# Kernel optimization log

Measured on AMD Instinct MI355X. Metric: run time of the kernel, lower is better.

Reference implementation:

```python
import jax, jax.numpy as jnp
import numpy as np


def setup_inputs() -> dict:
    key = jax.random.key(0)
    k1, k2, k3, k4, k5 = jax.random.split(key, 5)
    B, T, H_enc, H_dec, A = 64, 2048, 512, 512, 512
    scale_enc = float(np.sqrt(2.0 / (H_enc + A)))  # xavier_uniform-ish scale
    scale_dec = float(np.sqrt(2.0 / (H_dec + A)))
    scale_v = float(np.sqrt(2.0 / (A + 1)))
    return {
        "encoder_outputs": jax.random.normal(k1, (B, T, H_enc), dtype=jnp.float32),
        "decoder_hidden": jax.random.normal(k2, (B, H_dec), dtype=jnp.float32),
        "W_enc": jax.random.normal(k3, (A, H_enc), dtype=jnp.float32) * scale_enc,
        "W_dec": jax.random.normal(k4, (A, H_dec), dtype=jnp.float32) * scale_dec,
        "V": jax.random.normal(k5, (1, A), dtype=jnp.float32) * scale_v,
    }


def reference(encoder_outputs, decoder_hidden, W_enc, W_dec, V):
    # enc_proj: [B,T,A]; dec_proj: [B,1,A] broadcast-added
    enc_proj = jnp.einsum("bth,ah->bta", encoder_outputs, W_enc)
    dec_proj = jnp.einsum("bh,ah->ba", decoder_hidden, W_dec)[:, None, :]
    energy = jnp.tanh(enc_proj + dec_proj)                      # [B,T,A]
    scores = jnp.einsum("bta,a->bt", energy, V[0])              # [B,T]
    attention_weights = jax.nn.softmax(scores, axis=1)          # [B,T]
    context_vector = jnp.einsum("bt,bth->bh", attention_weights, encoder_outputs)
    return context_vector, attention_weights
```

## Files before the change

### kernel.cpp

```cpp
#include <hip/hip_runtime.h>

#define B_ 64
#define T_ 2048
#define H_ 512
#define A_ 512

typedef unsigned short u16;
typedef __attribute__((ext_vector_type(8))) short bf16x8;
typedef __attribute__((ext_vector_type(4))) float f32x4;

__device__ __forceinline__ u16 f2bf(float f) {
  unsigned u = __float_as_uint(f);
  unsigned r = (u + 0x7FFFu + ((u >> 16) & 1u)) >> 16;
  return (u16)r;
}

__device__ __forceinline__ float bf2f(u16 h) {
  return __uint_as_float(((unsigned)h) << 16);
}

__device__ __forceinline__ float fast_tanh(float x) {
  float e = __expf(2.0f * x);
  return 1.0f - 2.0f * __builtin_amdgcn_rcpf(e + 1.0f);
}

#define BAR_LDS() asm volatile("s_waitcnt lgkmcnt(0)\n\ts_barrier" ::: "memory")

__global__ void k_prep(const float* __restrict__ W, u16* __restrict__ wsB,
                       const float* __restrict__ dec, const float* __restrict__ Wd,
                       float* __restrict__ dp) {
  __shared__ float dl[H_];
  int tid = threadIdx.x;
  int bx = blockIdx.x;
  if (bx < 128) {
    int u = bx * 256 + tid;
    int a = u >> 6;
    int hq = u & 63;
    int ks = hq >> 2;
    int q = hq & 3;
    const float4* src = (const float4*)(W + a * H_ + hq * 8);
    float4 x0 = src[0], x1 = src[1];
    uint4 pk;
    pk.x = (unsigned)f2bf(x0.x) | ((unsigned)f2bf(x0.y) << 16);
    pk.y = (unsigned)f2bf(x0.z) | ((unsigned)f2bf(x0.w) << 16);
    pk.z = (unsigned)f2bf(x1.x) | ((unsigned)f2bf(x1.y) << 16);
    pk.w = (unsigned)f2bf(x1.z) | ((unsigned)f2bf(x1.w) << 16);
    int dst = ks * 2048 + (a >> 4) * 64 + q * 16 + (a & 15);
    ((uint4*)wsB)[dst] = pk;
  } else {
    int e = bx - 128;
    int b = e >> 3;
    int a0 = (e & 7) * 64;
    dl[tid] = dec[b * H_ + tid];
    dl[tid + 256] = dec[b * H_ + tid + 256];
    __syncthreads();
    int al = tid >> 2, p = tid & 3;
    const float4* wr = (const float4*)(Wd + (a0 + al) * H_ + p * 128);
    const float4* dv = (const float4*)(dl + p * 128);
    float s = 0.f;
#pragma unroll 8
    for (int i = 0; i < 32; ++i) {
      float4 w4 = wr[i], d4 = dv[i];
      s += w4.x * d4.x + w4.y * d4.y + w4.z * d4.z + w4.w * d4.w;
    }
    s += __shfl_xor(s, 1);
    s += __shfl_xor(s, 2);
    if (p == 0) dp[b * H_ + a0 + al] = s;
  }
}

__launch_bounds__(512, 4)
__global__ void k_scores(const float* __restrict__ enc, const u16* __restrict__ wsB,
                         const float* __restrict__ dpj, const float* __restrict__ V,
                         float* __restrict__ scores, float* __restrict__ part,
                         float* __restrict__ mz) {
  __shared__ __attribute__((aligned(16))) u16 Ab[64 * 512];
  __shared__ float red[8][64];
  int tid = threadIdx.x;
  int w = tid >> 6, l = tid & 63;
  int q = l >> 4, r = l & 15;
  int m0 = blockIdx.x * 64;
  int b = m0 >> 11;

  int rem = tid & 255;
  int sm = rem >> 6, sq = (rem >> 4) & 3, sr = rem & 15;
  const float* ab = enc + (size_t)(m0 + sm * 16 + sr) * H_ + (tid >> 8) * 32 + sq * 8;

#define LOADC(y0, y1, y2, y3, c)                                      \
  {                                                                   \
    y0 = *((const float4*)(ab + (2 * (c)) * 64));                     \
    y1 = *((const float4*)(ab + (2 * (c)) * 64 + 4));                 \
    y2 = *((const float4*)(ab + (2 * (c) + 1) * 64));                 \
    y3 = *((const float4*)(ab + (2 * (c) + 1) * 64 + 4));             \
  }
#define STG_WRITE(y0, y1, it)                                         \
  {                                                                   \
    uint4 pk;                                                         \
    pk.x = (unsigned)f2bf(y0.x) | ((unsigned)f2bf(y0.y) << 16);       \
    pk.y = (unsigned)f2bf(y0.z) | ((unsigned)f2bf(y0.w) << 16);       \
    pk.z = (unsigned)f2bf(y1.x) | ((unsigned)f2bf(y1.y) << 16);       \
    pk.w = (unsigned)f2bf(y1.z) | ((unsigned)f2bf(y1.w) << 16);       \
    ((uint4*)Ab)[(it) * 512 + tid] = pk;                              \
  }
#define WRITEC(y0, y1, y2, y3, c)                                     \
  {                                                                   \
    STG_WRITE(y0, y1, 2 * (c))                                        \
    STG_WRITE(y2, y3, 2 * (c) + 1)                                    \
  }
#define COMPUTE4(c)                                                   \
  {                                                                   \
    _Pragma("unroll") for (int kk = 0; kk < 4; ++kk) {                \
      int ks = (c) * 4 + kk;                                          \
      bf16x8 bb[4], af[4];                                            \
      _Pragma("unroll") for (int n = 0; n < 4; ++n)                   \
          bb[n] = bfrag[ks * 2048 + (w * 4 + n) * 64 + l];            \
      _Pragma("unroll") for (int m = 0; m < 4; ++m)                   \
          af[m] = *((const bf16x8*)&Ab[(ks * 256 + m * 64 + l) * 8]); \
      __builtin_amdgcn_s_setprio(1);                                  \
      _Pragma("unroll") for (int m = 0; m < 4; ++m)                   \
          _Pragma("unroll") for (int n = 0; n < 4; ++n)               \
              acc[m][n] = __builtin_amdgcn_mfma_f32_16x16x32_bf16(    \
                  af[m], bb[n], acc[m][n], 0, 0, 0);                  \
      __builtin_amdgcn_s_setprio(0);                                  \
    }                                                                 \
  }

  f32x4 acc[4][4];
#pragma unroll
  for (int m = 0; m < 4; ++m)
#pragma unroll
    for (int n = 0; n < 4; ++n) acc[m][n] = (f32x4){0.f, 0.f, 0.f, 0.f};

  const bf16x8* bfrag = (const bf16x8*)wsB;

  float4 ya0, ya1, ya2, ya3, yb0, yb1, yb2, yb3;
  LOADC(ya0, ya1, ya2, ya3, 0)
  LOADC(yb0, yb1, yb2, yb3, 1)
  WRITEC(ya0, ya1, ya2, ya3, 0)
  BAR_LDS();
  LOADC(ya0, ya1, ya2, ya3, 2)
  COMPUTE4(0)
  WRITEC(yb0, yb1, yb2, yb3, 1)
  BAR_LDS();
  LOADC(yb0, yb1, yb2, yb3, 3)
  COMPUTE4(1)
  WRITEC(ya0, ya1, ya2, ya3, 2)
  BAR_LDS();
  COMPUTE4(2)
  WRITEC(yb0, yb1, yb2, yb3, 3)
  BAR_LDS();
  COMPUTE4(3)

  float sp[4][4] = {};
  const float* db = dpj + b * A_;
#pragma unroll
  for (int n = 0; n < 4; ++n) {
    int col = w * 64 + n * 16 + r;
    float vv = V[col];
    float dd = db[col];
#pragma unroll
    for (int m = 0; m < 4; ++m)
#pragma unroll
      for (int j = 0; j < 4; ++j)
        sp[m][j] = fmaf(vv, fast_tanh(acc[m][n][j] + dd), sp[m][j]);
  }
#pragma unroll
  for (int m = 0; m < 4; ++m)
#pragma unroll
    for (int j = 0; j < 4; ++j) {
      float v = sp[m][j];
      v += __shfl_xor(v, 1);
      v += __shfl_xor(v, 2);
      v += __shfl_xor(v, 4);
      v += __shfl_xor(v, 8);
      sp[m][j] = v;
    }
  float outv = 0.f;
#pragma unroll
  for (int mm = 0; mm < 4; ++mm)
#pragma unroll
    for (int jj = 0; jj < 4; ++jj)
      if (r == mm * 4 + jj) outv = sp[mm][jj];
  red[w][(r >> 2) * 16 + q * 4 + (r & 3)] = outv;
  BAR_LDS();

  float s = 0.f;
#pragma unroll
  for (int ww = 0; ww < 8; ++ww) s += red[ww][l];
  if (w == 0) scores[m0 + l] = s;
  float mx = s;
#pragma unroll
  for (int off = 1; off <= 32; off <<= 1) mx = fmaxf(mx, __shfl_xor(mx, off));
  float e = __expf(s - mx);
  float Z = e;
#pragma unroll
  for (int off = 1; off <= 32; off <<= 1) Z += __shfl_xor(Z, off);
  if (tid == 0) {
    mz[blockIdx.x * 2] = mx;
    mz[blockIdx.x * 2 + 1] = Z;
  }
  float em[4];
#pragma unroll
  for (int m = 0; m < 4; ++m) em[m] = __shfl(e, m * 16 + r);

  {
    float pv0[8], pv1[8];
#pragma unroll
    for (int j = 0; j < 8; ++j) { pv0[j] = 0.f; pv1[j] = 0.f; }
#pragma unroll
    for (int ksl = 0; ksl < 2; ++ksl) {
      int ks = 2 * w + ksl;
#pragma unroll
      for (int m = 0; m < 4; ++m) {
        uint4 pk = ((const uint4*)Ab)[ks * 256 + m * 64 + l];
        float er = em[m];
        float v0 = bf2f((u16)(pk.x & 0xffff)), v1 = bf2f((u16)(pk.x >> 16));
        float v2 = bf2f((u16)(pk.y & 0xffff)), v3 = bf2f((u16)(pk.y >> 16));
        float v4 = bf2f((u16)(pk.z & 0xffff)), v5 = bf2f((u16)(pk.z >> 16));
        float v6 = bf2f((u16)(pk.w & 0xffff)), v7 = bf2f((u16)(pk.w >> 16));
        if (ksl == 0) {
          pv0[0] = fmaf(er, v0, pv0[0]); pv0[1] = fmaf(er, v1, pv0[1]);
          pv0[2] = fmaf(er, v2, pv0[2]); pv0[3] = fmaf(er, v3, pv0[3]);
          pv0[4] = fmaf(er, v4, pv0[4]); pv0[5] = fmaf(er, v5, pv0[5]);
          pv0[6] = fmaf(er, v6, pv0[6]); pv0[7] = fmaf(er, v7, pv0[7]);
        } else {
          pv1[0] = fmaf(er, v0, pv1[0]); pv1[1] = fmaf(er, v1, pv1[1]);
          pv1[2] = fmaf(er, v2, pv1[2]); pv1[3] = fmaf(er, v3, pv1[3]);
          pv1[4] = fmaf(er, v4, pv1[4]); pv1[5] = fmaf(er, v5, pv1[5]);
          pv1[6] = fmaf(er, v6, pv1[6]); pv1[7] = fmaf(er, v7, pv1[7]);
        }
      }
    }
#pragma unroll
    for (int j = 0; j < 8; ++j) {
      float a0 = pv0[j], a1 = pv1[j];
      a0 += __shfl_xor(a0, 1); a1 += __shfl_xor(a1, 1);
      a0 += __shfl_xor(a0, 2); a1 += __shfl_xor(a1, 2);
      a0 += __shfl_xor(a0, 4); a1 += __shfl_xor(a1, 4);
      a0 += __shfl_xor(a0, 8); a1 += __shfl_xor(a1, 8);
      pv0[j] = a0; pv1[j] = a1;
    }
    float ov = 0.f;
#pragma unroll
    for (int jj = 0; jj < 8; ++jj) {
      if (r == jj) ov = pv0[jj];
      if (r == jj + 8) ov = pv1[jj];
    }
    int col = w * 64 + (r >> 3) * 32 + q * 8 + (r & 7);
    part[(size_t)blockIdx.x * 512 + col] = ov;
  }
#undef LOADC
#undef STG_WRITE
#undef WRITEC
#undef COMPUTE4
}

__global__ void k_softmax(const float* __restrict__ scores, float* __restrict__ wts) {
  __shared__ float rm[4], rs[4];
  int b = blockIdx.x, tid = threadIdx.x;
  float s[8];
#pragma unroll
  for (int i = 0; i < 8; ++i) s[i] = scores[b * T_ + i * 256 + tid];
  float mx = s[0];
#pragma unroll
  for (int i = 1; i < 8; ++i) mx = fmaxf(mx, s[i]);
#pragma unroll
  for (int off = 1; off <= 32; off <<= 1) mx = fmaxf(mx, __shfl_xor(mx, off));
  if ((tid & 63) == 0) rm[tid >> 6] = mx;
  __syncthreads();
  mx = fmaxf(fmaxf(rm[0], rm[1]), fmaxf(rm[2], rm[3]));
  float ex[8], se = 0.f;
#pragma unroll
  for (int i = 0; i < 8; ++i) { ex[i] = __expf(s[i] - mx); se += ex[i]; }
#pragma unroll
  for (int off = 1; off <= 32; off <<= 1) se += __shfl_xor(se, off);
  if ((tid & 63) == 0) rs[tid >> 6] = se;
  __syncthreads();
  se = rs[0] + rs[1] + rs[2] + rs[3];
  float inv = 1.0f / se;
#pragma unroll
  for (int i = 0; i < 8; ++i) wts[b * T_ + i * 256 + tid] = ex[i] * inv;
}

__global__ void k_ctx_comb(const float* __restrict__ part, const float* __restrict__ mz,
                           float* __restrict__ ctx) {
  __shared__ float sM[32], sZ[32];
  int b = blockIdx.x, tid = threadIdx.x;
  if (tid < 32) {
    sM[tid] = mz[(b * 32 + tid) * 2];
    sZ[tid] = mz[(b * 32 + tid) * 2 + 1];
  }
  __syncthreads();
  float M = sM[0];
#pragma unroll
  for (int i = 1; i < 32; ++i) M = fmaxf(M, sM[i]);
  float denom = 0.f;
#pragma unroll
  for (int i = 0; i < 32; ++i) denom += sZ[i] * __expf(sM[i] - M);
  float s = 0.f;
#pragma unroll
  for (int i = 0; i < 32; ++i)
    s += part[((size_t)b * 32 + i) * 512 + tid] * __expf(sM[i] - M);
  ctx[b * 512 + tid] = s / denom;
}

extern "C" void kernel_launch(void* const* d_in, const int* in_sizes, int n_in,
                              void* d_out, int out_size, void* d_ws, size_t ws_size,
                              hipStream_t stream) {
  const float* enc  = (const float*)d_in[0];
  const float* dec  = (const float*)d_in[1];
  const float* Wenc = (const float*)d_in[2];
  const float* Wdec = (const float*)d_in[3];
  const float* V    = (const float*)d_in[4];
  float* out = (float*)d_out;
  char* ws = (char*)d_ws;

  u16* wsB      = (u16*)ws;
  float* dpj    = (float*)(ws + 512 * 1024);
  float* scores = (float*)(ws + 640 * 1024);
  float* part   = (float*)(ws + 1152 * 1024);
  float* mz     = (float*)(ws + 1152 * 1024 + 4 * 1024 * 1024);

  float* ctx = out;
  float* wts = out + B_ * H_;

  hipLaunchKernelGGL(k_prep, dim3(640), dim3(256), 0, stream, Wenc, wsB, dec, Wdec, dpj);
  hipLaunchKernelGGL(k_scores, dim3(2048), dim3(512), 0, stream, enc, wsB, dpj, V,
                     scores, part, mz);
  hipLaunchKernelGGL(k_softmax, dim3(64), dim3(256), 0, stream, scores, wts);
  hipLaunchKernelGGL(k_ctx_comb, dim3(64), dim3(512), 0, stream, part, mz, ctx);
}
```

Before: 122.0 us.

## Software-pipeline B fragment loads, use packed bf16 convert, butterfly reductions

The scores kernel now prefetches W fragments from global memory two k-steps ahead and interleaves LDS A loads with the MFMA groups, giving more register buffers per thread. The launch bound drops from 4 to 2 blocks per CU so the extra registers fit. Float-to-bf16 rounding now uses the hardware v_cvt_pk_bf16_f32 instruction instead of integer arithmetic, and tanh calls v_exp_f32 directly on a prescaled input. The shuffle reductions become recursive-halving butterflies, cutting the shuffle count at the cost of a permuted output index. The lower occupancy reduces the latency hiding available to the encoder streaming loads.

```diff
diff --git a/kernel.cpp b/kernel.cpp
--- a/kernel.cpp
+++ b/kernel.cpp
@@ -9,10 +9,10 @@
 typedef __attribute__((ext_vector_type(8))) short bf16x8;
 typedef __attribute__((ext_vector_type(4))) float f32x4;
 
-__device__ __forceinline__ u16 f2bf(float f) {
-  unsigned u = __float_as_uint(f);
-  unsigned r = (u + 0x7FFFu + ((u >> 16) & 1u)) >> 16;
-  return (u16)r;
+__device__ __forceinline__ unsigned cvtpk(float lo, float hi) {
+  unsigned d;
+  asm("v_cvt_pk_bf16_f32 %0, %1, %2" : "=v"(d) : "v"(lo), "v"(hi));
+  return d;
 }
 
 __device__ __forceinline__ float bf2f(u16 h) {
@@ -20,8 +20,9 @@
 }
 
 __device__ __forceinline__ float fast_tanh(float x) {
-  float e = __expf(2.0f * x);
-  return 1.0f - 2.0f * __builtin_amdgcn_rcpf(e + 1.0f);
+  float e2;
+  asm("v_exp_f32 %0, %1" : "=v"(e2) : "v"(x * 2.8853900817779268f));
+  return 1.0f - 2.0f * __builtin_amdgcn_rcpf(e2 + 1.0f);
 }
 
 #define BAR_LDS() asm volatile("s_waitcnt lgkmcnt(0)\n\ts_barrier" ::: "memory")
@@ -41,10 +42,10 @@
     const float4* src = (const float4*)(W + a * H_ + hq * 8);
     float4 x0 = src[0], x1 = src[1];
     uint4 pk;
-    pk.x = (unsigned)f2bf(x0.x) | ((unsigned)f2bf(x0.y) << 16);
-    pk.y = (unsigned)f2bf(x0.z) | ((unsigned)f2bf(x0.w) << 16);
-    pk.z = (unsigned)f2bf(x1.x) | ((unsigned)f2bf(x1.y) << 16);
-    pk.w = (unsigned)f2bf(x1.z) | ((unsigned)f2bf(x1.w) << 16);
+    pk.x = cvtpk(x0.x, x0.y);
+    pk.y = cvtpk(x0.z, x0.w);
+    pk.z = cvtpk(x1.x, x1.y);
+    pk.w = cvtpk(x1.z, x1.w);
     int dst = ks * 2048 + (a >> 4) * 64 + q * 16 + (a & 15);
     ((uint4*)wsB)[dst] = pk;
   } else {
@@ -69,7 +70,7 @@
   }
 }
 
-__launch_bounds__(512, 4)
+__launch_bounds__(512, 2)
 __global__ void k_scores(const float* __restrict__ enc, const u16* __restrict__ wsB,
                          const float* __restrict__ dpj, const float* __restrict__ V,
                          float* __restrict__ scores, float* __restrict__ part,
@@ -86,112 +87,123 @@
   int sm = rem >> 6, sq = (rem >> 4) & 3, sr = rem & 15;
   const float* ab = enc + (size_t)(m0 + sm * 16 + sr) * H_ + (tid >> 8) * 32 + sq * 8;
 
-#define LOADC(y0, y1, y2, y3, c)                                      \
-  {                                                                   \
-    y0 = *((const float4*)(ab + (2 * (c)) * 64));                     \
-    y1 = *((const float4*)(ab + (2 * (c)) * 64 + 4));                 \
-    y2 = *((const float4*)(ab + (2 * (c) + 1) * 64));                 \
-    y3 = *((const float4*)(ab + (2 * (c) + 1) * 64 + 4));             \
-  }
-#define STG_WRITE(y0, y1, it)                                         \
-  {                                                                   \
-    uint4 pk;                                                         \
-    pk.x = (unsigned)f2bf(y0.x) | ((unsigned)f2bf(y0.y) << 16);       \
-    pk.y = (unsigned)f2bf(y0.z) | ((unsigned)f2bf(y0.w) << 16);       \
-    pk.z = (unsigned)f2bf(y1.x) | ((unsigned)f2bf(y1.y) << 16);       \
-    pk.w = (unsigned)f2bf(y1.z) | ((unsigned)f2bf(y1.w) << 16);       \
-    ((uint4*)Ab)[(it) * 512 + tid] = pk;                              \
-  }
-#define WRITEC(y0, y1, y2, y3, c)                                     \
-  {                                                                   \
-    STG_WRITE(y0, y1, 2 * (c))                                        \
-    STG_WRITE(y2, y3, 2 * (c) + 1)                                    \
-  }
-#define COMPUTE4(c)                                                   \
-  {                                                                   \
-    _Pragma("unroll") for (int kk = 0; kk < 4; ++kk) {                \
-      int ks = (c) * 4 + kk;                                          \
-      bf16x8 bb[4], af[4];                                            \
-      _Pragma("unroll") for (int n = 0; n < 4; ++n)                   \
-          bb[n] = bfrag[ks * 2048 + (w * 4 + n) * 64 + l];            \
-      _Pragma("unroll") for (int m = 0; m < 4; ++m)                   \
-          af[m] = *((const bf16x8*)&Ab[(ks * 256 + m * 64 + l) * 8]); \
-      __builtin_amdgcn_s_setprio(1);                                  \
-      _Pragma("unroll") for (int m = 0; m < 4; ++m)                   \
-          _Pragma("unroll") for (int n = 0; n < 4; ++n)               \
-              acc[m][n] = __builtin_amdgcn_mfma_f32_16x16x32_bf16(    \
-                  af[m], bb[n], acc[m][n], 0, 0, 0);                  \
-      __builtin_amdgcn_s_setprio(0);                                  \
-    }                                                                 \
-  }
-
-  f32x4 acc[4][4];
-#pragma unroll
-  for (int m = 0; m < 4; ++m)
-#pragma unroll
-    for (int n = 0; n < 4; ++n) acc[m][n] = (f32x4){0.f, 0.f, 0.f, 0.f};
-
-  const bf16x8* bfrag = (const bf16x8*)wsB;
-
-  float4 ya0, ya1, ya2, ya3, yb0, yb1, yb2, yb3;
-  LOADC(ya0, ya1, ya2, ya3, 0)
-  LOADC(yb0, yb1, yb2, yb3, 1)
-  WRITEC(ya0, ya1, ya2, ya3, 0)
-  BAR_LDS();
-  LOADC(ya0, ya1, ya2, ya3, 2)
-  COMPUTE4(0)
-  WRITEC(yb0, yb1, yb2, yb3, 1)
-  BAR_LDS();
-  LOADC(yb0, yb1, yb2, yb3, 3)
-  COMPUTE4(1)
-  WRITEC(ya0, ya1, ya2, ya3, 2)
-  BAR_LDS();
-  COMPUTE4(2)
-  WRITEC(yb0, yb1, yb2, yb3, 3)
-  BAR_LDS();
-  COMPUTE4(3)
-
-  float sp[4][4] = {};
+  float vv[4], dd[4];
   const float* db = dpj + b * A_;
 #pragma unroll
   for (int n = 0; n < 4; ++n) {
     int col = w * 64 + n * 16 + r;
-    float vv = V[col];
-    float dd = db[col];
+    vv[n] = V[col];
+    dd[n] = db[col];
+  }
+
+  const bf16x8* bfrag = (const bf16x8*)wsB;
+
+#define LOADC(P, c)                                                     \
+  { P##0 = *((const float4*)(ab + (2 * (c)) * 64));                     \
+    P##1 = *((const float4*)(ab + (2 * (c)) * 64 + 4));                 \
+    P##2 = *((const float4*)(ab + (2 * (c) + 1) * 64));                 \
+    P##3 = *((const float4*)(ab + (2 * (c) + 1) * 64 + 4)); }
+#define WRITEC(P, c)                                                    \
+  { uint4 k0, k1;                                                       \
+    k0.x = cvtpk((P##0).x, (P##0).y); k0.y = cvtpk((P##0).z, (P##0).w); \
+    k0.z = cvtpk((P##1).x, (P##1).y); k0.w = cvtpk((P##1).z, (P##1).w); \
+    k1.x = cvtpk((P##2).x, (P##2).y); k1.y = cvtpk((P##2).z, (P##2).w); \
+    k1.z = cvtpk((P##3).x, (P##3).y); k1.w = cvtpk((P##3).z, (P##3).w); \
+    ((uint4*)Ab)[(2 * (c)) * 512 + tid] = k0;                           \
+    ((uint4*)Ab)[(2 * (c) + 1) * 512 + tid] = k1; }
+#define LOADB(dst, ks)                                                  \
+  { _Pragma("unroll") for (int n = 0; n < 4; ++n)                       \
+      dst[n] = bfrag[(ks) * 2048 + (w * 4 + n) * 64 + l]; }
+#define LOADA(dst, ks)                                                  \
+  { _Pragma("unroll") for (int m = 0; m < 4; ++m)                       \
+      dst[m] = *((const bf16x8*)&Ab[((ks) * 256 + m * 64 + l) * 8]); }
+#define MFMA16(af, bb)                                                  \
+  { __builtin_amdgcn_s_setprio(1);                                      \
+    _Pragma("unroll") for (int m = 0; m < 4; ++m)                       \
+      _Pragma("unroll") for (int n = 0; n < 4; ++n)                     \
+        acc[m][n] = __builtin_amdgcn_mfma_f32_16x16x32_bf16(            \
+            af[m], bb[n], acc[m][n], 0, 0, 0);                          \
+    __builtin_amdgcn_s_setprio(0); }
+#define CHUNK(c, PF3)                                                   \
+  { LOADA(aA, 4 * (c));                                                 \
+    LOADB(s2, 4 * (c) + 2)                                              \
+    LOADA(aB, 4 * (c) + 1);                                             \
+    MFMA16(aA, s0)                                                      \
+    LOADB(s3, 4 * (c) + 3)                                              \
+    LOADA(aA, 4 * (c) + 2);                                             \
+    MFMA16(aB, s1)                                                      \
+    if (PF3) LOADB(s0, 4 * (c) + 4)                                     \
+    LOADA(aB, 4 * (c) + 3);                                             \
+    MFMA16(aA, s2)                                                      \
+    if (PF3) LOADB(s1, 4 * (c) + 5)                                     \
+    MFMA16(aB, s3) }
+
+  f32x4 acc[4][4];
+#pragma unroll
+  for (int m = 0; m < 4; ++m)
+#pragma unroll
+    for (int n = 0; n < 4; ++n) acc[m][n] = (f32x4){0.f, 0.f, 0.f, 0.f};
+
+  float4 pa0, pa1, pa2, pa3, pb0, pb1, pb2, pb3;
+  bf16x8 s0[4], s1[4], s2[4], s3[4], aA[4], aB[4];
+
+  LOADC(pa, 0)
+  LOADC(pb, 1)
+  LOADB(s0, 0)
+  LOADB(s1, 1)
+  WRITEC(pa, 0)
+  BAR_LDS();
+  LOADC(pa, 2)
+  CHUNK(0, true)
+  WRITEC(pb, 1)
+  BAR_LDS();
+  LOADC(pb, 3)
+  CHUNK(1, true)
+  WRITEC(pa, 2)
+  BAR_LDS();
+  CHUNK(2, true)
+  WRITEC(pb, 3)
+  BAR_LDS();
+  CHUNK(3, false)
+
+  float sp[16];
+#pragma unroll
+  for (int i = 0; i < 16; ++i) sp[i] = 0.f;
+#pragma unroll
+  for (int n = 0; n < 4; ++n) {
 #pragma unroll
     for (int m = 0; m < 4; ++m)
 #pragma unroll
       for (int j = 0; j < 4; ++j)
-        sp[m][j] = fmaf(vv, fast_tanh(acc[m][n][j] + dd), sp[m][j]);
-  }
-#pragma unroll
-  for (int m = 0; m < 4; ++m)
-#pragma unroll
-    for (int j = 0; j < 4; ++j) {
-      float v = sp[m][j];
-      v += __shfl_xor(v, 1);
-      v += __shfl_xor(v, 2);
-      v += __shfl_xor(v, 4);
-      v += __shfl_xor(v, 8);
-      sp[m][j] = v;
+        sp[m * 4 + j] = fmaf(vv[n], fast_tanh(acc[m][n][j] + dd[n]), sp[m * 4 + j]);
+  }
+#pragma unroll
+  for (int st = 0; st < 4; ++st) {
+    const int s = 1 << st;
+    const int cnt = 16 >> (st + 1);
+    bool hi = (r & s) != 0;
+#pragma unroll
+    for (int i = 0; i < cnt; ++i) {
+      float a = hi ? sp[i + cnt] : sp[i];
+      float bs = hi ? sp[i] : sp[i + cnt];
+      sp[i] = a + __shfl_xor(bs, s);
     }
-  float outv = 0.f;
-#pragma unroll
-  for (int mm = 0; mm < 4; ++mm)
-#pragma unroll
-    for (int jj = 0; jj < 4; ++jj)
-      if (r == mm * 4 + jj) outv = sp[mm][jj];
-  red[w][(r >> 2) * 16 + q * 4 + (r & 3)] = outv;
-  BAR_LDS();
-
-  float s = 0.f;
-#pragma unroll
-  for (int ww = 0; ww < 8; ++ww) s += red[ww][l];
-  if (w == 0) scores[m0 + l] = s;
-  float mx = s;
+  }
+  {
+    int i4 = ((r & 1) << 3) | ((r & 2) << 1) | ((r & 4) >> 1) | ((r & 8) >> 3);
+    BAR_LDS();
+    red[w][(i4 >> 2) * 16 + q * 4 + (i4 & 3)] = sp[0];
+  }
+  BAR_LDS();
+
+  float s_ = 0.f;
+#pragma unroll
+  for (int ww = 0; ww < 8; ++ww) s_ += red[ww][l];
+  if (w == 0) scores[m0 + l] = s_;
+  float mx = s_;
 #pragma unroll
   for (int off = 1; off <= 32; off <<= 1) mx = fmaxf(mx, __shfl_xor(mx, off));
-  float e = __expf(s - mx);
+  float e = __expf(s_ - mx);
   float Z = e;
 #pragma unroll
   for (int off = 1; off <= 32; off <<= 1) Z += __shfl_xor(Z, off);
@@ -209,10 +221,10 @@
     for (int j = 0; j < 8; ++j) { pv0[j] = 0.f; pv1[j] = 0.f; }
 #pragma unroll
     for (int ksl = 0; ksl < 2; ++ksl) {
-      int ks = 2 * w + ksl;
+      int ks_ = 2 * w + ksl;
 #pragma unroll
       for (int m = 0; m < 4; ++m) {
-        uint4 pk = ((const uint4*)Ab)[ks * 256 + m * 64 + l];
+        uint4 pk = ((const uint4*)Ab)[ks_ * 256 + m * 64 + l];
         float er = em[m];
         float v0 = bf2f((u16)(pk.x & 0xffff)), v1 = bf2f((u16)(pk.x >> 16));
         float v2 = bf2f((u16)(pk.y & 0xffff)), v3 = bf2f((u16)(pk.y >> 16));
@@ -232,27 +244,34 @@
       }
     }
 #pragma unroll
-    for (int j = 0; j < 8; ++j) {
-      float a0 = pv0[j], a1 = pv1[j];
-      a0 += __shfl_xor(a0, 1); a1 += __shfl_xor(a1, 1);
-      a0 += __shfl_xor(a0, 2); a1 += __shfl_xor(a1, 2);
-      a0 += __shfl_xor(a0, 4); a1 += __shfl_xor(a1, 4);
-      a0 += __shfl_xor(a0, 8); a1 += __shfl_xor(a1, 8);
-      pv0[j] = a0; pv1[j] = a1;
+    for (int st = 0; st < 3; ++st) {
+      const int s = 1 << st;
+      const int cnt = 8 >> (st + 1);
+      bool hi = (r & s) != 0;
+#pragma unroll
+      for (int i = 0; i < cnt; ++i) {
+        float a0 = hi ? pv0[i + cnt] : pv0[i];
+        float b0 = hi ? pv0[i] : pv0[i + cnt];
+        pv0[i] = a0 + __shfl_xor(b0, s);
+        float a1 = hi ? pv1[i + cnt] : pv1[i];
+        float b1 = hi ? pv1[i] : pv1[i + cnt];
+        pv1[i] = a1 + __shfl_xor(b1, s);
+      }
     }
-    float ov = 0.f;
-#pragma unroll
-    for (int jj = 0; jj < 8; ++jj) {
-      if (r == jj) ov = pv0[jj];
-      if (r == jj + 8) ov = pv1[jj];
-    }
-    int col = w * 64 + (r >> 3) * 32 + q * 8 + (r & 7);
+    bool h8 = (r & 8) != 0;
+    float va = h8 ? pv1[0] : pv0[0];
+    float vb = h8 ? pv0[0] : pv1[0];
+    float ov = va + __shfl_xor(vb, 8);
+    int g3 = ((r & 1) << 2) | (r & 2) | ((r & 4) >> 2);
+    int col = w * 64 + (h8 ? 32 : 0) + q * 8 + g3;
     part[(size_t)blockIdx.x * 512 + col] = ov;
   }
 #undef LOADC
-#undef STG_WRITE
 #undef WRITEC
-#undef COMPUTE4
+#undef LOADB
+#undef LOADA
+#undef MFMA16
+#undef CHUNK
 }
 
 __global__ void k_softmax(const float* __restrict__ scores, float* __restrict__ wts) {
```

Result: slower. 164.8 us (+35.1%).
